# Performance work log

Hardware: AMD Instinct MI355X
Metric: run time of the kernel (lower is better)

## Reference

```python
import jax, jax.numpy as jnp
import numpy as np

TAU = 1.0
EPS_MASS = 1e-6
EPS_LOG = 1e-8
EPS_DEN = 1e-8


def setup_inputs() -> dict:
    key = jax.random.key(0)
    k1, k2, k3, k4 = jax.random.split(key, 4)
    B, T, P, D, R, K = 4, 1024, 16, 64, 32, 64
    m = jax.random.normal(k1, (B, T, P, D), dtype=jnp.float32)
    w = jax.random.uniform(k2, (B, T, P), dtype=jnp.float32)
    p = jax.random.uniform(k3, (B, T, P, K), dtype=jnp.float32)
    patch_centers = jax.random.normal(k4, (R, D), dtype=jnp.float32)
    return {"m": m, "w": w, "p": p, "patch_centers": patch_centers}


def reference(m, w, p, patch_centers):
    # m: [B,T,P,D], w: [B,T,P], p: [B,T,P,K], patch_centers: [R,D]
    R = patch_centers.shape[0]
    # squared distances patch-component -> center: [B,T,P,R]
    diff = m[..., None, :] - patch_centers  # [B,T,P,R,D]
    dists = jnp.sum(diff * diff, axis=-1)
    gamma = jax.nn.softmax(-dists / TAU, axis=-1)  # [B,T,P,R]
    start_mass = gamma * w[..., None]  # [B,T,P,R]
    total_mass_r = start_mass.sum(axis=2)  # [B,T,R]
    p_bar_num = jnp.einsum('btpk,btpr->btrk', p, start_mass)  # [B,T,R,K]
    p_bar = p_bar_num / (total_mass_r[..., None] + EPS_MASS)
    # pairwise center affinity omega: [R,R]
    cdiff = patch_centers[:, None, :] - patch_centers[None, :, :]
    center_dists = jnp.sum(cdiff * cdiff, axis=-1)
    omega = jnp.exp(-center_dists / TAU)
    # pairwise JS divergence over K: [B,T,R,R]
    p_r = p_bar[:, :, :, None, :]  # [B,T,R,1,K]
    p_s = p_bar[:, :, None, :, :]  # [B,T,1,R,K]
    m_dist = 0.5 * (p_r + p_s)
    log_m = jnp.log(m_dist + EPS_LOG)
    kl_r = jnp.sum(p_r * (jnp.log(p_r + EPS_LOG) - log_m), axis=-1)
    kl_s = jnp.sum(p_s * (jnp.log(p_s + EPS_LOG) - log_m), axis=-1)
    js_rs = 0.5 * (kl_r + kl_s)  # [B,T,R,R]
    weighted_js = omega * js_rs
    mask = jnp.triu(jnp.ones((R, R), dtype=jnp.float32), k=1)
    loss = jnp.sum(weighted_js * mask) / (jnp.sum(mask) + EPS_DEN)
    return loss
```

## Files before the change

kernel.cpp:

```cpp
#include <hip/hip_runtime.h>

#define PP 16
#define DD 64
#define RR 32
#define KK 64
#define NBT 4096

#define LOG2E 1.4426950408889634f
#define LN2   0.6931471805599453f
#define D2_CUT 25.0f

static __device__ __forceinline__ float fast_log2(float x) { return __builtin_amdgcn_logf(x); }
static __device__ __forceinline__ float fast_exp2(float x) { return __builtin_amdgcn_exp2f(x); }
static __device__ __forceinline__ float fast_rcp(float x)  { return __builtin_amdgcn_rcpf(x); }

#define WAVE_SYNC() asm volatile("s_waitcnt lgkmcnt(0)" ::: "memory")

__global__ __launch_bounds__(1024) void prune_kernel(const float* __restrict__ c,
                                                     float* __restrict__ cc,
                                                     int* __restrict__ npairs,
                                                     float2* __restrict__ plist) {
    __shared__ float2 sm_cT2[32 * 33];
    __shared__ float red[16];
    __shared__ float dmin_sh;
    __shared__ int cnt;
    const int t = threadIdx.x;

    {
        const float2* c2 = (const float2*)c;
        int rr = t >> 5, d2i = t & 31;
        sm_cT2[d2i * 33 + rr] = c2[t];
    }
    if (t == 0) cnt = 0;
    __syncthreads();

    const int r = t >> 5, s = t & 31;
    const bool active = s > r;
    float d2 = 0.f;
#pragma unroll
    for (int i = 0; i < 32; ++i) {
        float2 ca = sm_cT2[i * 33 + r];
        float2 cb = sm_cT2[i * 33 + s];
        float dx = ca.x - cb.x, dy = ca.y - cb.y;
        d2 = fmaf(dx, dx, d2);
        d2 = fmaf(dy, dy, d2);
    }
    float dm = active ? d2 : 3.4e38f;
#pragma unroll
    for (int off = 32; off > 0; off >>= 1) dm = fminf(dm, __shfl_down(dm, off, 64));
    if ((t & 63) == 0) red[t >> 6] = dm;
    __syncthreads();
    if (t < 64) {
        float v = (t < 16) ? red[t] : 3.4e38f;
#pragma unroll
        for (int off = 8; off > 0; off >>= 1) v = fminf(v, __shfl_down(v, off, 64));
        if (t == 0) dmin_sh = v;
    }
    if (t < RR) {
        float a2 = 0.f;
#pragma unroll
        for (int i = 0; i < 32; ++i) {
            float2 cv = sm_cT2[i * 33 + t];
            a2 = fmaf(cv.x, cv.x, a2);
            a2 = fmaf(cv.y, cv.y, a2);
        }
        cc[t] = a2;
    }
    __syncthreads();
    const float dmin = dmin_sh;
    if (active && d2 <= dmin + D2_CUT) {
        int idx = atomicAdd(&cnt, 1);
        plist[idx] = make_float2(fast_exp2(-d2 * LOG2E), __int_as_float(t));
    }
    __syncthreads();
    if (t == 0) *npairs = cnt;
}

__global__ __launch_bounds__(256, 3) void sheaf3_kernel(
    const float* __restrict__ m, const float* __restrict__ w,
    const float* __restrict__ p, const float* __restrict__ c,
    const float* __restrict__ cc, const int* __restrict__ npairs,
    const float2* __restrict__ plist, float* __restrict__ partials) {
    __shared__ float2 sm_cT2[32 * 33];
    __shared__ __align__(16) float sm_pl[4][2048];
    __shared__ __align__(16) float sm_scr[4][640];
    __shared__ float sm_sw4[4][16];

    const int tid = threadIdx.x;
    const int wv  = tid >> 6;
    const int ln  = tid & 63;
    const int bt  = blockIdx.x * 4 + wv;

    float* pl  = sm_pl[wv];
    float* scr = sm_scr[wv];
    float* swv = sm_sw4[wv];

    const int r_ = ln & 31, h_ = ln >> 5;
    const int k  = ln;

    const float* pg_ = p + (size_t)bt * PP * KK + k;
    float pcol[PP];
#pragma unroll
    for (int pi = 0; pi < PP; ++pi) pcol[pi] = pg_[pi * KK];
    const int np = __builtin_amdgcn_readfirstlane(*npairs);
    const float ccr  = cc[r_];
    const float wreg = w[(size_t)bt * PP + (ln >> 2)];

    {
        const float2* c2 = (const float2*)c;
#pragma unroll
        for (int it = 0; it < 4; ++it) {
            int idx = tid + 256 * it;
            sm_cT2[(idx & 31) * 33 + (idx >> 5)] = c2[idx];
        }
        const float4* m4g = (const float4*)(m + (size_t)bt * PP * DD);
        float4* m4l = (float4*)pl;
#pragma unroll
        for (int it = 0; it < 4; ++it) m4l[ln + 64 * it] = m4g[ln + 64 * it];
    }
    __syncthreads();

    {
        const float* mw = pl;
        float acc[8] = {0.f, 0.f, 0.f, 0.f, 0.f, 0.f, 0.f, 0.f};
#pragma unroll
        for (int d4 = 0; d4 < 16; ++d4) {
            float2 ca = sm_cT2[(2 * d4) * 33 + r_];
            float2 cb = sm_cT2[(2 * d4 + 1) * 33 + r_];
#pragma unroll
            for (int i = 0; i < 8; ++i) {
                float4 mm = *(const float4*)(mw + (h_ * 8 + i) * DD + d4 * 4);
                acc[i] = fmaf(mm.x, ca.x, acc[i]);
                acc[i] = fmaf(mm.y, ca.y, acc[i]);
                acc[i] = fmaf(mm.z, cb.x, acc[i]);
                acc[i] = fmaf(mm.w, cb.y, acc[i]);
            }
        }
#pragma unroll
        for (int i = 0; i < 8; ++i)
            scr[(h_ * 8 + i) * 36 + r_] = fmaf(2.f, acc[i], -ccr);
    }
    WAVE_SYNC();

    {
        const int pq = ln >> 2, q = ln & 3;
        float4 v0 = *(const float4*)(scr + pq * 36 + q * 8);
        float4 v1 = *(const float4*)(scr + pq * 36 + q * 8 + 4);
        float mx = fmaxf(fmaxf(fmaxf(v0.x, v0.y), fmaxf(v0.z, v0.w)),
                         fmaxf(fmaxf(v1.x, v1.y), fmaxf(v1.z, v1.w)));
        mx = fmaxf(mx, __shfl_xor(mx, 1, 64));
        mx = fmaxf(mx, __shfl_xor(mx, 2, 64));
        v0.x = fast_exp2((v0.x - mx) * LOG2E); v0.y = fast_exp2((v0.y - mx) * LOG2E);
        v0.z = fast_exp2((v0.z - mx) * LOG2E); v0.w = fast_exp2((v0.w - mx) * LOG2E);
        v1.x = fast_exp2((v1.x - mx) * LOG2E); v1.y = fast_exp2((v1.y - mx) * LOG2E);
        v1.z = fast_exp2((v1.z - mx) * LOG2E); v1.w = fast_exp2((v1.w - mx) * LOG2E);
        float ssum = ((v0.x + v0.y) + (v0.z + v0.w)) + ((v1.x + v1.y) + (v1.z + v1.w));
        ssum += __shfl_xor(ssum, 1, 64);
        ssum += __shfl_xor(ssum, 2, 64);
        *(float4*)(scr + pq * 36 + q * 8)     = v0;
        *(float4*)(scr + pq * 36 + q * 8 + 4) = v1;
        if (q == 0) swv[pq] = wreg * fast_rcp(ssum);
    }
    WAVE_SYNC();

    {
        float ef[8];
        float tot = 0.f;
#pragma unroll
        for (int i = 0; i < 8; ++i) {
            ef[i] = scr[(h_ * 8 + i) * 36 + r_] * swv[h_ * 8 + i];
            tot += ef[i];
        }
        tot += __shfl_xor(tot, 32, 64);
        float inv = fast_rcp(tot + 1e-6f);
#pragma unroll
        for (int i = 0; i < 8; ++i)
            scr[r_ * 20 + h_ * 8 + i] = ef[i] * inv;
    }
    WAVE_SYNC();

    {
#pragma unroll
        for (int r = 0; r < 32; ++r) {
            const float4* mt = (const float4*)(scr + r * 20);
            float4 a0 = mt[0], a1 = mt[1], a2 = mt[2], a3 = mt[3];
            float pb = 0.f;
            pb = fmaf(pcol[0],  a0.x, pb); pb = fmaf(pcol[1],  a0.y, pb);
            pb = fmaf(pcol[2],  a0.z, pb); pb = fmaf(pcol[3],  a0.w, pb);
            pb = fmaf(pcol[4],  a1.x, pb); pb = fmaf(pcol[5],  a1.y, pb);
            pb = fmaf(pcol[6],  a1.z, pb); pb = fmaf(pcol[7],  a1.w, pb);
            pb = fmaf(pcol[8],  a2.x, pb); pb = fmaf(pcol[9],  a2.y, pb);
            pb = fmaf(pcol[10], a2.z, pb); pb = fmaf(pcol[11], a2.w, pb);
            pb = fmaf(pcol[12], a3.x, pb); pb = fmaf(pcol[13], a3.y, pb);
            pb = fmaf(pcol[14], a3.z, pb); pb = fmaf(pcol[15], a3.w, pb);
            pl[r * KK + k] = pb;
        }
    }
    WAVE_SYNC();

    {
        float acc = 0.f;
        for (int i = 0; i < np; ++i) {
            float2 e = plist[i];
            int rs = __float_as_int(e.y);
            float pa  = pl[(rs >> 5) * KK + k];
            float pbv = pl[(rs & 31) * KK + k];
            float sum = pa + pbv;
            float la = fast_log2(pa + 1e-8f);
            float lb = fast_log2(pbv + 1e-8f);
            float lm = fast_log2(fmaf(0.5f, sum, 1e-8f));
            float t = fmaf(pa, la, fmaf(pbv, lb, -sum * lm));
            acc = fmaf(e.x, t, acc);
        }
#pragma unroll
        for (int off = 32; off > 0; off >>= 1) acc += __shfl_down(acc, off, 64);
        if (k == 0) partials[bt] = acc * (0.5f * LN2 / 496.0f);
    }
}

__global__ __launch_bounds__(256) void reduce_kernel(const float* __restrict__ partials,
                                                     float* __restrict__ out) {
    __shared__ float sred[4];
    const int tid = threadIdx.x;
    const float4* p4 = (const float4*)partials;
    float acc = 0.f;
#pragma unroll
    for (int i = 0; i < 4; ++i) {
        float4 v = p4[tid + 256 * i];
        acc += (v.x + v.y) + (v.z + v.w);
    }
#pragma unroll
    for (int off = 32; off > 0; off >>= 1) acc += __shfl_down(acc, off, 64);
    if ((tid & 63) == 0) sred[tid >> 6] = acc;
    __syncthreads();
    if (tid == 0) out[0] = (sred[0] + sred[1]) + (sred[2] + sred[3]);
}

extern "C" void kernel_launch(void* const* d_in, const int* in_sizes, int n_in,
                              void* d_out, int out_size, void* d_ws, size_t ws_size,
                              hipStream_t stream) {
    const float* m = (const float*)d_in[0];
    const float* w = (const float*)d_in[1];
    const float* p = (const float*)d_in[2];
    const float* c = (const float*)d_in[3];
    float* out = (float*)d_out;

    float* wsf      = (float*)d_ws;
    int*   npairs   = (int*)d_ws;
    float* cc       = wsf + 64;
    float2* plist   = (float2*)(wsf + 128);
    float* partials = wsf + 2048;

    prune_kernel<<<1, 1024, 0, stream>>>(c, cc, npairs, plist);
    sheaf3_kernel<<<NBT / 4, 256, 0, stream>>>(m, w, p, c, cc, npairs, plist, partials);
    reduce_kernel<<<1, 256, 0, stream>>>(partials, out);
}
```

Measured before the change: 100.0 us.

## Read m directly from global, broadcast gamma via readlane, unroll JS loop by two

The kernel no longer stages m into shared memory and reads it straight from global memory inside the distance dot product. The normalized gamma weights stay in registers and are broadcast across lanes with readlane for the p_bar contraction, which removes a shared-memory transpose and one wave sync. The pairwise JS loop is unrolled by two to expose more independent log and LDS work. In exchange, the global loads of m are repeated across lanes and may hit cache less efficiently, and 512 readlane instructions go through the scalar path.

```diff
diff --git a/kernel.cpp b/kernel.cpp
--- a/kernel.cpp
+++ b/kernel.cpp
@@ -13,6 +13,9 @@
 static __device__ __forceinline__ float fast_log2(float x) { return __builtin_amdgcn_logf(x); }
 static __device__ __forceinline__ float fast_exp2(float x) { return __builtin_amdgcn_exp2f(x); }
 static __device__ __forceinline__ float fast_rcp(float x)  { return __builtin_amdgcn_rcpf(x); }
+static __device__ __forceinline__ float lane_bcast(float x, int lane) {
+    return __int_as_float(__builtin_amdgcn_readlane(__float_as_int(x), lane));
+}
 
 #define WAVE_SYNC() asm volatile("s_waitcnt lgkmcnt(0)" ::: "memory")
 
@@ -76,7 +79,7 @@
     if (t == 0) *npairs = cnt;
 }
 
-__global__ __launch_bounds__(256, 3) void sheaf3_kernel(
+__global__ __launch_bounds__(256, 3) void sheaf4_kernel(
     const float* __restrict__ m, const float* __restrict__ w,
     const float* __restrict__ p, const float* __restrict__ c,
     const float* __restrict__ cc, const int* __restrict__ npairs,
@@ -113,15 +116,11 @@
             int idx = tid + 256 * it;
             sm_cT2[(idx & 31) * 33 + (idx >> 5)] = c2[idx];
         }
+    }
+    __syncthreads();
+
+    {
         const float4* m4g = (const float4*)(m + (size_t)bt * PP * DD);
-        float4* m4l = (float4*)pl;
-#pragma unroll
-        for (int it = 0; it < 4; ++it) m4l[ln + 64 * it] = m4g[ln + 64 * it];
-    }
-    __syncthreads();
-
-    {
-        const float* mw = pl;
         float acc[8] = {0.f, 0.f, 0.f, 0.f, 0.f, 0.f, 0.f, 0.f};
 #pragma unroll
         for (int d4 = 0; d4 < 16; ++d4) {
@@ -129,7 +128,7 @@
             float2 cb = sm_cT2[(2 * d4 + 1) * 33 + r_];
 #pragma unroll
             for (int i = 0; i < 8; ++i) {
-                float4 mm = *(const float4*)(mw + (h_ * 8 + i) * DD + d4 * 4);
+                float4 mm = m4g[(h_ * 8 + i) * 16 + d4];
                 acc[i] = fmaf(mm.x, ca.x, acc[i]);
                 acc[i] = fmaf(mm.y, ca.y, acc[i]);
                 acc[i] = fmaf(mm.z, cb.x, acc[i]);
@@ -163,8 +162,8 @@
     }
     WAVE_SYNC();
 
-    {
-        float ef[8];
+    float ef[8];
+    {
         float tot = 0.f;
 #pragma unroll
         for (int i = 0; i < 8; ++i) {
@@ -174,42 +173,54 @@
         tot += __shfl_xor(tot, 32, 64);
         float inv = fast_rcp(tot + 1e-6f);
 #pragma unroll
-        for (int i = 0; i < 8; ++i)
-            scr[r_ * 20 + h_ * 8 + i] = ef[i] * inv;
+        for (int i = 0; i < 8; ++i) ef[i] *= inv;
+    }
+
+    {
+#pragma unroll
+        for (int r = 0; r < 32; ++r) {
+            float pb = 0.f;
+#pragma unroll
+            for (int i = 0; i < 8; ++i) {
+                pb = fmaf(lane_bcast(ef[i], r),      pcol[i],     pb);
+                pb = fmaf(lane_bcast(ef[i], r + 32), pcol[8 + i], pb);
+            }
+            pl[r * KK + k] = pb;
+        }
     }
     WAVE_SYNC();
 
     {
-#pragma unroll
-        for (int r = 0; r < 32; ++r) {
-            const float4* mt = (const float4*)(scr + r * 20);
-            float4 a0 = mt[0], a1 = mt[1], a2 = mt[2], a3 = mt[3];
-            float pb = 0.f;
-            pb = fmaf(pcol[0],  a0.x, pb); pb = fmaf(pcol[1],  a0.y, pb);
-            pb = fmaf(pcol[2],  a0.z, pb); pb = fmaf(pcol[3],  a0.w, pb);
-            pb = fmaf(pcol[4],  a1.x, pb); pb = fmaf(pcol[5],  a1.y, pb);
-            pb = fmaf(pcol[6],  a1.z, pb); pb = fmaf(pcol[7],  a1.w, pb);
-            pb = fmaf(pcol[8],  a2.x, pb); pb = fmaf(pcol[9],  a2.y, pb);
-            pb = fmaf(pcol[10], a2.z, pb); pb = fmaf(pcol[11], a2.w, pb);
-            pb = fmaf(pcol[12], a3.x, pb); pb = fmaf(pcol[13], a3.y, pb);
-            pb = fmaf(pcol[14], a3.z, pb); pb = fmaf(pcol[15], a3.w, pb);
-            pl[r * KK + k] = pb;
-        }
-    }
-    WAVE_SYNC();
-
-    {
         float acc = 0.f;
-        for (int i = 0; i < np; ++i) {
+        int i = 0;
+        for (; i + 1 < np; i += 2) {
+            float2 e0 = plist[i];
+            float2 e1 = plist[i + 1];
+            int rs0 = __float_as_int(e0.y);
+            int rs1 = __float_as_int(e1.y);
+            float pa0 = pl[(rs0 >> 5) * KK + k];
+            float pb0 = pl[(rs0 & 31) * KK + k];
+            float pa1 = pl[(rs1 >> 5) * KK + k];
+            float pb1 = pl[(rs1 & 31) * KK + k];
+            float s0 = pa0 + pb0, s1 = pa1 + pb1;
+            float t0 = fmaf(pa0, fast_log2(pa0 + 1e-8f),
+                       fmaf(pb0, fast_log2(pb0 + 1e-8f),
+                            -s0 * fast_log2(fmaf(0.5f, s0, 1e-8f))));
+            float t1 = fmaf(pa1, fast_log2(pa1 + 1e-8f),
+                       fmaf(pb1, fast_log2(pb1 + 1e-8f),
+                            -s1 * fast_log2(fmaf(0.5f, s1, 1e-8f))));
+            acc = fmaf(e0.x, t0, acc);
+            acc = fmaf(e1.x, t1, acc);
+        }
+        if (i < np) {
             float2 e = plist[i];
             int rs = __float_as_int(e.y);
             float pa  = pl[(rs >> 5) * KK + k];
             float pbv = pl[(rs & 31) * KK + k];
             float sum = pa + pbv;
-            float la = fast_log2(pa + 1e-8f);
-            float lb = fast_log2(pbv + 1e-8f);
-            float lm = fast_log2(fmaf(0.5f, sum, 1e-8f));
-            float t = fmaf(pa, la, fmaf(pbv, lb, -sum * lm));
+            float t = fmaf(pa, fast_log2(pa + 1e-8f),
+                      fmaf(pbv, fast_log2(pbv + 1e-8f),
+                           -sum * fast_log2(fmaf(0.5f, sum, 1e-8f))));
             acc = fmaf(e.x, t, acc);
         }
 #pragma unroll
@@ -252,6 +263,6 @@
     float* partials = wsf + 2048;
 
     prune_kernel<<<1, 1024, 0, stream>>>(c, cc, npairs, plist);
-    sheaf3_kernel<<<NBT / 4, 256, 0, stream>>>(m, w, p, c, cc, npairs, plist, partials);
+    sheaf4_kernel<<<NBT / 4, 256, 0, stream>>>(m, w, p, c, cc, npairs, plist, partials);
     reduce_kernel<<<1, 256, 0, stream>>>(partials, out);
 }
```

Result: slower. 107.6 us (+7.6%).
